# Kernel optimization log

Hardware: AMD Instinct MI355X
Metric: run time of the kernel (lower is better)

## Reference

```python
import jax, jax.numpy as jnp
import numpy as np

N, E, C, L, OUT = 50000, 600000, 128, 2, 64


def setup_inputs() -> dict:
    key = jax.random.key(0)
    ks = jax.random.split(key, 8)
    s = 1.0 / np.sqrt(C)
    return {
        "x": jax.random.normal(ks[0], (N, C), jnp.float32),
        "edge_index": jax.random.randint(ks[1], (2, E), 0, N, jnp.int64),
        "W_neigh": jax.random.normal(ks[2], (L, C, C), jnp.float32) * s,
        "W_root": jax.random.normal(ks[3], (L, C, C), jnp.float32) * s,
        "b_conv": jnp.zeros((L, C), jnp.float32),
        "ln_gamma": jnp.ones((L, C), jnp.float32),
        "ln_beta": jnp.zeros((L, C), jnp.float32),
        "W_head": jax.random.normal(ks[4], (OUT, C), jnp.float32) * s,
        "b_head": jnp.zeros((OUT,), jnp.float32),
        "num_seed": 1024,
    }


def _layernorm(h, g, b, eps=1e-5):
    mu = jnp.mean(h, axis=-1, keepdims=True)
    var = jnp.mean(jnp.square(h - mu), axis=-1, keepdims=True)
    return (h - mu) * jax.lax.rsqrt(var + eps) * g + b


def reference(x, edge_index, W_neigh, W_root, b_conv, ln_gamma, ln_beta, W_head, b_head, num_seed):
    src, dst = edge_index[0], edge_index[1]
    n = x.shape[0]
    # in-degree for mean aggregation (clamped to 1 as in PyG mean aggr)
    deg = jax.ops.segment_sum(jnp.ones((src.shape[0],), x.dtype), dst, num_segments=n)
    inv_deg = 1.0 / jnp.maximum(deg, 1.0)  # [N]
    for l in range(W_neigh.shape[0]):
        agg = jax.ops.segment_sum(x[src], dst, num_segments=n) * inv_deg[:, None]  # [N,C]
        h = agg @ W_neigh[l].T + x @ W_root[l].T + b_conv[l]
        x = jax.nn.relu(_layernorm(h, ln_gamma[l], ln_beta[l]))
    # head on the seed nodes (entity table slice starts at 0 here)
    return x[:num_seed] @ W_head.T + b_head
```

## Files before the change

kernel.cpp:

```cpp
#include <hip/hip_runtime.h>

#define C 128

typedef __attribute__((ext_vector_type(8))) short short8;
typedef __attribute__((ext_vector_type(16))) float floatx16;

__device__ __forceinline__ unsigned short f2b(float f) {
    union { float f; unsigned u; } v; v.f = f;
    unsigned u = v.u + 0x7fffu + ((v.u >> 16) & 1u);
    return (unsigned short)(u >> 16);
}
__device__ __forceinline__ void acc_pair(unsigned u, float& lo, float& hi) {
    union { unsigned u; float f; } a, b;
    a.u = u << 16;
    b.u = u & 0xffff0000u;
    lo += a.f;
    hi += b.f;
}

__global__ void cast_mark_count_kernel(const float* __restrict__ x, unsigned short* __restrict__ xb, int n4x,
                                       const float* __restrict__ Wn, unsigned short* __restrict__ Wnb,
                                       const float* __restrict__ Wr, unsigned short* __restrict__ Wrb, int n4w,
                                       const float* __restrict__ Wh, unsigned short* __restrict__ Whb, int n4h,
                                       const int* __restrict__ src, const int* __restrict__ dst,
                                       int* __restrict__ deg, int* __restrict__ needed,
                                       int E, int num_seed,
                                       int castBlocks) {
    if ((int)blockIdx.x < castBlocks) {
        int i = blockIdx.x * blockDim.x + threadIdx.x;
        const float* in;
        unsigned short* out;
        int idx;
        if (i < n4x) { in = x; out = xb; idx = i; }
        else if (i < n4x + n4w) { in = Wn; out = Wnb; idx = i - n4x; }
        else if (i < n4x + 2 * n4w) { in = Wr; out = Wrb; idx = i - n4x - n4w; }
        else if (i < n4x + 2 * n4w + n4h) { in = Wh; out = Whb; idx = i - n4x - 2 * n4w; }
        else return;
        float4 v = ((const float4*)in)[idx];
        ushort4 o;
        o.x = f2b(v.x); o.y = f2b(v.y); o.z = f2b(v.z); o.w = f2b(v.w);
        ((ushort4*)out)[idx] = o;
    } else {
        int e = (blockIdx.x - castBlocks) * blockDim.x + threadIdx.x;
        if (e < num_seed) needed[e] = 1;
        if (e < E) {
            int d = dst[e];
            atomicAdd(&deg[d], 1);
            if (d < num_seed) needed[src[e]] = 1;
        }
    }
}

__global__ void scan_fused_kernel(const int* __restrict__ deg, const int* __restrict__ needed,
                                  unsigned long long* __restrict__ status, int* __restrict__ counter,
                                  int* __restrict__ row_start, int* __restrict__ cursor,
                                  int* __restrict__ nodelist, int* __restrict__ Mptr, int n) {
    __shared__ int smD[256];
    __shared__ int smN[256];
    __shared__ int sbid, sprefD, sprefN;
    int t = threadIdx.x;
    if (t == 0) sbid = atomicAdd(counter, 1);
    __syncthreads();
    int bid = sbid;
    int i = bid * 256 + t;
    int d = (i < n) ? deg[i] : 0;
    int nd = (i < n) ? needed[i] : 0;
    smD[t] = d; smN[t] = nd;
    __syncthreads();
    for (int off = 1; off < 256; off <<= 1) {
        int vD = (t >= off) ? smD[t - off] : 0;
        int vN = (t >= off) ? smN[t - off] : 0;
        __syncthreads();
        smD[t] += vD; smN[t] += vN;
        __syncthreads();
    }
    int totD = smD[255], totN = smN[255];
    if (t == 0) {
        if (bid == 0) {
            atomicExch(&status[0],
                       (2ULL << 62) | ((unsigned long long)(unsigned)totN << 32) | (unsigned)totD);
            sprefD = 0; sprefN = 0;
        } else {
            atomicExch(&status[bid],
                       (1ULL << 62) | ((unsigned long long)(unsigned)totN << 32) | (unsigned)totD);
            int accD = 0, accN = 0;
            for (int j = bid - 1; j >= 0;) {
                unsigned long long v = atomicAdd(&status[j], 0ULL);
                unsigned f = (unsigned)(v >> 62);
                if (f == 0) { __builtin_amdgcn_s_sleep(1); continue; }
                accD += (int)(unsigned)(v & 0xffffffffULL);
                accN += (int)((v >> 32) & 0x3fffffffULL);
                if (f == 2) break;
                --j;
            }
            atomicExch(&status[bid],
                       (2ULL << 62) | ((unsigned long long)(unsigned)(accN + totN) << 32) |
                           (unsigned)(accD + totD));
            sprefD = accD; sprefN = accN;
        }
    }
    __syncthreads();
    int exD = smD[t] - d + sprefD;
    int exN = smN[t] - nd + sprefN;
    if (i < n) {
        row_start[i] = exD;
        cursor[i] = exD;
        if (nd) nodelist[exN] = i;
        if (i == n - 1) { row_start[n] = exD + d; *Mptr = exN + nd; }
    }
}

__global__ void bucket_kernel(const int* __restrict__ src, const int* __restrict__ dst,
                              int* __restrict__ cursor, int* __restrict__ esrc, int E,
                              const int* __restrict__ needed) {
    int e = blockIdx.x * blockDim.x + threadIdx.x;
    if (e < E) {
        int d = dst[e];
        if (needed[d]) {
            int p = atomicAdd(&cursor[d], 1);
            esrc[p] = src[e];
        }
    }
}

__global__ void aggregate_kernel(const unsigned short* __restrict__ xb, const int* __restrict__ row_start,
                                 const int* __restrict__ esrc,
                                 unsigned short* __restrict__ agg, int n,
                                 const int* __restrict__ nodelist, const int* __restrict__ Mptr) {
    int wid = (blockIdx.x * blockDim.x + threadIdx.x) >> 6;
    int lane = threadIdx.x & 63;
    int q = lane >> 4, l16 = lane & 15;
    int qb = lane & 48;
    int pos = wid * 4 + q;
    int m = Mptr ? *Mptr : n;
    if (pos >= m) return;
    int node = nodelist ? nodelist[pos] : pos;

    int beg = row_start[node];
    int end = row_start[node + 1];
    size_t choff = (size_t)l16 * 8;

    float a0 = 0.f, a1 = 0.f, a2 = 0.f, a3 = 0.f, a4 = 0.f, a5 = 0.f, a6 = 0.f, a7 = 0.f;

    for (int base = beg; base < end; base += 16) {
        int cnt = min(end - base, 16);
        int e_val = (base + l16 < end) ? esrc[base + l16] : 0;
        int j = 0;
        for (; j + 8 <= cnt; j += 8) {
            int s0 = __shfl(e_val, qb | j, 64);
            int s1 = __shfl(e_val, qb | (j + 1), 64);
            int s2 = __shfl(e_val, qb | (j + 2), 64);
            int s3 = __shfl(e_val, qb | (j + 3), 64);
            int s4 = __shfl(e_val, qb | (j + 4), 64);
            int s5 = __shfl(e_val, qb | (j + 5), 64);
            int s6 = __shfl(e_val, qb | (j + 6), 64);
            int s7 = __shfl(e_val, qb | (j + 7), 64);
            uint4 v0 = *(const uint4*)(xb + (size_t)s0 * C + choff);
            uint4 v1 = *(const uint4*)(xb + (size_t)s1 * C + choff);
            uint4 v2 = *(const uint4*)(xb + (size_t)s2 * C + choff);
            uint4 v3 = *(const uint4*)(xb + (size_t)s3 * C + choff);
            uint4 v4 = *(const uint4*)(xb + (size_t)s4 * C + choff);
            uint4 v5 = *(const uint4*)(xb + (size_t)s5 * C + choff);
            uint4 v6 = *(const uint4*)(xb + (size_t)s6 * C + choff);
            uint4 v7 = *(const uint4*)(xb + (size_t)s7 * C + choff);
            acc_pair(v0.x, a0, a1); acc_pair(v0.y, a2, a3); acc_pair(v0.z, a4, a5); acc_pair(v0.w, a6, a7);
            acc_pair(v1.x, a0, a1); acc_pair(v1.y, a2, a3); acc_pair(v1.z, a4, a5); acc_pair(v1.w, a6, a7);
            acc_pair(v2.x, a0, a1); acc_pair(v2.y, a2, a3); acc_pair(v2.z, a4, a5); acc_pair(v2.w, a6, a7);
            acc_pair(v3.x, a0, a1); acc_pair(v3.y, a2, a3); acc_pair(v3.z, a4, a5); acc_pair(v3.w, a6, a7);
            acc_pair(v4.x, a0, a1); acc_pair(v4.y, a2, a3); acc_pair(v4.z, a4, a5); acc_pair(v4.w, a6, a7);
            acc_pair(v5.x, a0, a1); acc_pair(v5.y, a2, a3); acc_pair(v5.z, a4, a5); acc_pair(v5.w, a6, a7);
            acc_pair(v6.x, a0, a1); acc_pair(v6.y, a2, a3); acc_pair(v6.z, a4, a5); acc_pair(v6.w, a6, a7);
            acc_pair(v7.x, a0, a1); acc_pair(v7.y, a2, a3); acc_pair(v7.z, a4, a5); acc_pair(v7.w, a6, a7);
        }
        for (; j + 4 <= cnt; j += 4) {
            int s0 = __shfl(e_val, qb | j, 64);
            int s1 = __shfl(e_val, qb | (j + 1), 64);
            int s2 = __shfl(e_val, qb | (j + 2), 64);
            int s3 = __shfl(e_val, qb | (j + 3), 64);
            uint4 v0 = *(const uint4*)(xb + (size_t)s0 * C + choff);
            uint4 v1 = *(const uint4*)(xb + (size_t)s1 * C + choff);
            uint4 v2 = *(const uint4*)(xb + (size_t)s2 * C + choff);
            uint4 v3 = *(const uint4*)(xb + (size_t)s3 * C + choff);
            acc_pair(v0.x, a0, a1); acc_pair(v0.y, a2, a3); acc_pair(v0.z, a4, a5); acc_pair(v0.w, a6, a7);
            acc_pair(v1.x, a0, a1); acc_pair(v1.y, a2, a3); acc_pair(v1.z, a4, a5); acc_pair(v1.w, a6, a7);
            acc_pair(v2.x, a0, a1); acc_pair(v2.y, a2, a3); acc_pair(v2.z, a4, a5); acc_pair(v2.w, a6, a7);
            acc_pair(v3.x, a0, a1); acc_pair(v3.y, a2, a3); acc_pair(v3.z, a4, a5); acc_pair(v3.w, a6, a7);
        }
        for (; j < cnt; ++j) {
            int s0 = __shfl(e_val, qb | j, 64);
            uint4 v0 = *(const uint4*)(xb + (size_t)s0 * C + choff);
            acc_pair(v0.x, a0, a1); acc_pair(v0.y, a2, a3); acc_pair(v0.z, a4, a5); acc_pair(v0.w, a6, a7);
        }
    }

    float sc = 1.0f / fmaxf((float)(end - beg), 1.0f);
    uint4 o;
    o.x = ((unsigned)f2b(a1 * sc) << 16) | (unsigned)f2b(a0 * sc);
    o.y = ((unsigned)f2b(a3 * sc) << 16) | (unsigned)f2b(a2 * sc);
    o.z = ((unsigned)f2b(a5 * sc) << 16) | (unsigned)f2b(a4 * sc);
    o.w = ((unsigned)f2b(a7 * sc) << 16) | (unsigned)f2b(a6 * sc);
    *(uint4*)(agg + (size_t)pos * C + choff) = o;
}

__launch_bounds__(256)
__global__ void gemm_mfma_ln_relu_kernel(const unsigned short* __restrict__ Aagg,
                                         const unsigned short* __restrict__ Xin,
                                         const unsigned short* __restrict__ Wn,
                                         const unsigned short* __restrict__ Wr,
                                         const float* __restrict__ bconv, const float* __restrict__ gamma,
                                         const float* __restrict__ beta, unsigned short* __restrict__ Xout,
                                         int n,
                                         const int* __restrict__ nodelist, const int* __restrict__ Mptr,
                                         const unsigned short* __restrict__ Whb,
                                         const float* __restrict__ bh, float* __restrict__ out) {
    __shared__ unsigned short Xs[64][136];
    __shared__ unsigned short Ws[128][136];
    __shared__ float Ls[64][2];
    __shared__ float Lss[64][2];

    int m = Mptr ? *Mptr : n;
    int row0 = blockIdx.x * 64;
    if (row0 >= m) return;

    int tid = threadIdx.x;
    int wave = tid >> 6, lane = tid & 63;
    int rh = wave & 1, ch = wave >> 1;
    int l31 = lane & 31, half = lane >> 5;

    floatx16 acc0, acc1;
#pragma unroll
    for (int i = 0; i < 16; ++i) { acc0[i] = 0.f; acc1[i] = 0.f; }

#pragma unroll
    for (int phase = 0; phase < 2; ++phase) {
        const unsigned short* Ap = phase ? Xin : Aagg;
        const unsigned short* Wp = phase ? Wr : Wn;
        __syncthreads();
#pragma unroll
        for (int i = 0; i < 4; ++i) {
            int cidx = tid + 256 * i;
            int r = cidx >> 4, koff = (cidx & 15) * 8;
            uint4 v = make_uint4(0u, 0u, 0u, 0u);
            int rg = row0 + r;
            if (rg < m) {
                int rowid = (phase && nodelist) ? nodelist[rg] : rg;
                v = *(const uint4*)(Ap + (size_t)rowid * C + koff);
            }
            *(uint4*)&Xs[r][koff] = v;
        }
#pragma unroll
        for (int i = 0; i < 8; ++i) {
            int cidx = tid + 256 * i;
            int r = cidx >> 4, koff = (cidx & 15) * 8;
            uint4 v = *(const uint4*)(Wp + (size_t)r * C + koff);
            *(uint4*)&Ws[r][koff] = v;
        }
        __syncthreads();
#pragma unroll
        for (int kc = 0; kc < C; kc += 16) {
            int ko = kc + half * 8;
            short8 a = *(const short8*)&Xs[rh * 32 + l31][ko];
            short8 b0 = *(const short8*)&Ws[ch * 64 + l31][ko];
            short8 b1 = *(const short8*)&Ws[ch * 64 + 32 + l31][ko];
            acc0 = __builtin_amdgcn_mfma_f32_32x32x16_bf16(a, b0, acc0, 0, 0, 0);
            acc1 = __builtin_amdgcn_mfma_f32_32x32x16_bf16(a, b1, acc1, 0, 0, 0);
        }
    }

    int col0 = ch * 64 + l31;
    int col1 = col0 + 32;
    float bc0 = bconv[col0], bc1 = bconv[col1];
#pragma unroll
    for (int r = 0; r < 16; ++r) {
        float h0 = acc0[r] + bc0;
        float h1 = acc1[r] + bc1;
        float s = h0 + h1, ss = h0 * h0 + h1 * h1;
#pragma unroll
        for (int mk = 1; mk < 32; mk <<= 1) {
            s += __shfl_xor(s, mk, 64);
            ss += __shfl_xor(ss, mk, 64);
        }
        if (l31 == 0) {
            int row_l = rh * 32 + (r & 3) + 8 * (r >> 2) + 4 * half;
            Ls[row_l][ch] = s;
            Lss[row_l][ch] = ss;
        }
    }
    __syncthreads();

    if (Whb) {
#pragma unroll
        for (int i = 0; i < 4; ++i) {
            int cidx = tid + 256 * i;
            int r = cidx >> 4, koff = (cidx & 15) * 8;
            uint4 v = *(const uint4*)(Whb + (size_t)r * C + koff);
            *(uint4*)&Ws[r][koff] = v;
        }
    }

    float g0 = gamma[col0], g1 = gamma[col1];
    float be0 = beta[col0], be1 = beta[col1];
#pragma unroll
    for (int r = 0; r < 16; ++r) {
        int row_l = rh * 32 + (r & 3) + 8 * (r >> 2) + 4 * half;
        float s = Ls[row_l][0] + Ls[row_l][1];
        float ss = Lss[row_l][0] + Lss[row_l][1];
        float mu = s * (1.0f / 128.0f);
        float var = ss * (1.0f / 128.0f) - mu * mu;
        float rs = rsqrtf(var + 1e-5f);
        float h0 = acc0[r] + bc0;
        float h1 = acc1[r] + bc1;
        float o0 = fmaxf((h0 - mu) * rs * g0 + be0, 0.f);
        float o1 = fmaxf((h1 - mu) * rs * g1 + be1, 0.f);
        Xs[row_l][col0] = f2b(o0);
        Xs[row_l][col1] = f2b(o1);
    }
    __syncthreads();

    if (Whb) {
        floatx16 hc;
#pragma unroll
        for (int i = 0; i < 16; ++i) hc[i] = 0.f;
        int m0 = rh * 32, n0 = ch * 32;
#pragma unroll
        for (int kc = 0; kc < C; kc += 16) {
            int ko = kc + half * 8;
            short8 a = *(const short8*)&Xs[m0 + l31][ko];
            short8 b = *(const short8*)&Ws[n0 + l31][ko];
            hc = __builtin_amdgcn_mfma_f32_32x32x16_bf16(a, b, hc, 0, 0, 0);
        }
        int oc = n0 + l31;
        float bhv = bh[oc];
#pragma unroll
        for (int r = 0; r < 16; ++r) {
            int row_l = m0 + (r & 3) + 8 * (r >> 2) + 4 * half;
            int rg = row0 + row_l;
            if (rg < m) out[(size_t)rg * 64 + oc] = hc[r] + bhv;
        }
    } else {
#pragma unroll
        for (int i = 0; i < 4; ++i) {
            int cidx = tid + 256 * i;
            int r = cidx >> 4, koff = (cidx & 15) * 8;
            int rg = row0 + r;
            if (rg < m) {
                int orow = nodelist ? nodelist[rg] : rg;
                *(uint4*)(Xout + (size_t)orow * C + koff) = *(const uint4*)&Xs[r][koff];
            }
        }
    }
}

extern "C" void kernel_launch(void* const* d_in, const int* in_sizes, int n_in,
                              void* d_out, int out_size, void* d_ws, size_t ws_size,
                              hipStream_t stream) {
    const float* x = (const float*)d_in[0];
    const int* ei = (const int*)d_in[1];
    const float* Wn = (const float*)d_in[2];
    const float* Wr = (const float*)d_in[3];
    const float* bconv = (const float*)d_in[4];
    const float* gamma = (const float*)d_in[5];
    const float* beta = (const float*)d_in[6];
    const float* Wh = (const float*)d_in[7];
    const float* bh = (const float*)d_in[8];

    int N = in_sizes[0] / C;
    int E = in_sizes[1] / 2;
    int L = in_sizes[2] / (C * C);
    int num_seed = out_size / 64;
    int nchunks = (N + 255) / 256;

    char* ws = (char*)d_ws;
    size_t off = 0;
    auto alloc = [&](size_t bytes) {
        void* p = ws + off;
        off = (off + bytes + 255) & ~(size_t)255;
        return p;
    };
    int* deg = (int*)alloc((size_t)N * 4);
    int* needed = (int*)alloc((size_t)N * 4);
    int* counter = (int*)alloc(256);
    unsigned long long* status = (unsigned long long*)alloc((size_t)nchunks * 8);
    size_t zero_span = off;
    int* row_start = (int*)alloc((size_t)(N + 1) * 4);
    int* cursor = (int*)alloc((size_t)N * 4);
    int* nodelist = (int*)alloc((size_t)N * 4);
    int* Mptr = (int*)alloc(4);
    int* esrc = (int*)alloc((size_t)E * 4);
    unsigned short* xb = (unsigned short*)alloc((size_t)N * C * 2);
    unsigned short* aggb = (unsigned short*)alloc((size_t)N * C * 2);
    unsigned short* xA = (unsigned short*)alloc((size_t)N * C * 2);
    unsigned short* xB = (unsigned short*)alloc((size_t)N * C * 2);
    unsigned short* Wnb = (unsigned short*)alloc((size_t)L * C * C * 2);
    unsigned short* Wrb = (unsigned short*)alloc((size_t)L * C * C * 2);
    unsigned short* Whb = (unsigned short*)alloc((size_t)64 * C * 2);

    const int* srcIdx = ei;
    const int* dstIdx = ei + E;

    int n4x = N * C / 4;
    int n4w = L * C * C / 4;
    int n4h = 64 * C / 4;
    int castBlocks = (n4x + 2 * n4w + n4h + 255) / 256;
    int degBlocks = (max(E, num_seed) + 255) / 256;

    hipMemsetAsync(ws, 0, zero_span, stream);
    cast_mark_count_kernel<<<castBlocks + degBlocks, 256, 0, stream>>>(
        x, xb, n4x, Wn, Wnb, Wr, Wrb, n4w, Wh, Whb, n4h,
        srcIdx, dstIdx, deg, needed, E, num_seed, castBlocks);
    scan_fused_kernel<<<nchunks, 256, 0, stream>>>(deg, needed, status, counter,
                                                   row_start, cursor, nodelist, Mptr, N);
    bucket_kernel<<<(E + 255) / 256, 256, 0, stream>>>(srcIdx, dstIdx, cursor, esrc, E, needed);

    const unsigned short* cur = xb;
    unsigned short* bufs[2] = {xA, xB};
    for (int l = 0; l < L; ++l) {
        bool last = (l == L - 1);
        bool front = !last && (l == L - 2);
        int nl = last ? num_seed : N;
        const int* list = front ? nodelist : nullptr;
        const int* Mp = front ? Mptr : nullptr;
        unsigned short* nxt = bufs[l & 1];
        int aggThreads = ((nl + 3) / 4) * 64;
        aggregate_kernel<<<(aggThreads + 255) / 256, 256, 0, stream>>>(
            cur, row_start, esrc, aggb, nl, list, Mp);
        gemm_mfma_ln_relu_kernel<<<(nl + 63) / 64, 256, 0, stream>>>(
            aggb, cur, Wnb + (size_t)l * C * C, Wrb + (size_t)l * C * C,
            bconv + (size_t)l * C, gamma + (size_t)l * C, beta + (size_t)l * C, nxt, nl,
            list, Mp,
            last ? Whb : (const unsigned short*)nullptr, bh, (float*)d_out);
        cur = nxt;
    }
}
```

Baseline: 181.0 us.

## Fuse all stages into one persistent kernel with software grid barriers

Replaces the sequence of separate launches (cast/count, decoupled-lookback scan, bucket, per-layer aggregate and GEMM) with a single persistent kernel of 512 blocks. The blocks synchronise through atomic-counter grid barriers and use grid-stride loops. The scan becomes a two-pass reduce-then-scan over block sums. The goal is to remove launch gaps and tail effects between the small stages. In exchange it relies on all 512 blocks being co-resident, adds barrier spin cost, and may lose per-stage occupancy because shared memory is sized for the GEMM throughout.

```diff
diff --git a/kernel.cpp b/kernel.cpp
--- a/kernel.cpp
+++ b/kernel.cpp
@@ -1,6 +1,7 @@
 #include <hip/hip_runtime.h>
 
 #define C 128
+#define NB 512
 
 typedef __attribute__((ext_vector_type(8))) short short8;
 typedef __attribute__((ext_vector_type(16))) float floatx16;
@@ -18,210 +19,104 @@
     hi += b.f;
 }
 
-__global__ void cast_mark_count_kernel(const float* __restrict__ x, unsigned short* __restrict__ xb, int n4x,
-                                       const float* __restrict__ Wn, unsigned short* __restrict__ Wnb,
-                                       const float* __restrict__ Wr, unsigned short* __restrict__ Wrb, int n4w,
-                                       const float* __restrict__ Wh, unsigned short* __restrict__ Whb, int n4h,
-                                       const int* __restrict__ src, const int* __restrict__ dst,
-                                       int* __restrict__ deg, int* __restrict__ needed,
-                                       int E, int num_seed,
-                                       int castBlocks) {
-    if ((int)blockIdx.x < castBlocks) {
-        int i = blockIdx.x * blockDim.x + threadIdx.x;
-        const float* in;
-        unsigned short* out;
-        int idx;
-        if (i < n4x) { in = x; out = xb; idx = i; }
-        else if (i < n4x + n4w) { in = Wn; out = Wnb; idx = i - n4x; }
-        else if (i < n4x + 2 * n4w) { in = Wr; out = Wrb; idx = i - n4x - n4w; }
-        else if (i < n4x + 2 * n4w + n4h) { in = Wh; out = Whb; idx = i - n4x - 2 * n4w; }
-        else return;
-        float4 v = ((const float4*)in)[idx];
-        ushort4 o;
-        o.x = f2b(v.x); o.y = f2b(v.y); o.z = f2b(v.z); o.w = f2b(v.w);
-        ((ushort4*)out)[idx] = o;
-    } else {
-        int e = (blockIdx.x - castBlocks) * blockDim.x + threadIdx.x;
-        if (e < num_seed) needed[e] = 1;
-        if (e < E) {
-            int d = dst[e];
-            atomicAdd(&deg[d], 1);
-            if (d < num_seed) needed[src[e]] = 1;
-        }
-    }
-}
-
-__global__ void scan_fused_kernel(const int* __restrict__ deg, const int* __restrict__ needed,
-                                  unsigned long long* __restrict__ status, int* __restrict__ counter,
-                                  int* __restrict__ row_start, int* __restrict__ cursor,
-                                  int* __restrict__ nodelist, int* __restrict__ Mptr, int n) {
-    __shared__ int smD[256];
-    __shared__ int smN[256];
-    __shared__ int sbid, sprefD, sprefN;
-    int t = threadIdx.x;
-    if (t == 0) sbid = atomicAdd(counter, 1);
+__device__ __forceinline__ void gbar(int* bar, int idx) {
     __syncthreads();
-    int bid = sbid;
-    int i = bid * 256 + t;
-    int d = (i < n) ? deg[i] : 0;
-    int nd = (i < n) ? needed[i] : 0;
-    smD[t] = d; smN[t] = nd;
+    if (threadIdx.x == 0) {
+        int* c = bar + idx * 64;
+        __threadfence();
+        __hip_atomic_fetch_add(c, 1, __ATOMIC_RELEASE, __HIP_MEMORY_SCOPE_AGENT);
+        while (__hip_atomic_load(c, __ATOMIC_ACQUIRE, __HIP_MEMORY_SCOPE_AGENT) < NB)
+            __builtin_amdgcn_s_sleep(8);
+        __threadfence();
+    }
     __syncthreads();
-    for (int off = 1; off < 256; off <<= 1) {
-        int vD = (t >= off) ? smD[t - off] : 0;
-        int vN = (t >= off) ? smN[t - off] : 0;
-        __syncthreads();
-        smD[t] += vD; smN[t] += vN;
-        __syncthreads();
-    }
-    int totD = smD[255], totN = smN[255];
-    if (t == 0) {
-        if (bid == 0) {
-            atomicExch(&status[0],
-                       (2ULL << 62) | ((unsigned long long)(unsigned)totN << 32) | (unsigned)totD);
-            sprefD = 0; sprefN = 0;
-        } else {
-            atomicExch(&status[bid],
-                       (1ULL << 62) | ((unsigned long long)(unsigned)totN << 32) | (unsigned)totD);
-            int accD = 0, accN = 0;
-            for (int j = bid - 1; j >= 0;) {
-                unsigned long long v = atomicAdd(&status[j], 0ULL);
-                unsigned f = (unsigned)(v >> 62);
-                if (f == 0) { __builtin_amdgcn_s_sleep(1); continue; }
-                accD += (int)(unsigned)(v & 0xffffffffULL);
-                accN += (int)((v >> 32) & 0x3fffffffULL);
-                if (f == 2) break;
-                --j;
+}
+
+__device__ __forceinline__ void agg_phase(const unsigned short* __restrict__ xb,
+                                          const int* __restrict__ row_start,
+                                          const int* __restrict__ esrc,
+                                          unsigned short* __restrict__ agg, int m,
+                                          const int* __restrict__ nodelist) {
+    int tid = threadIdx.x;
+    int lane = tid & 63;
+    int q = lane >> 4, l16 = lane & 15, qb = lane & 48;
+    int wid = blockIdx.x * 4 + (tid >> 6);
+    size_t choff = (size_t)l16 * 8;
+
+    for (int pos = wid * 4 + q; pos < m; pos += NB * 16) {
+        int node = nodelist ? nodelist[pos] : pos;
+        int beg = row_start[node];
+        int end = row_start[node + 1];
+        float a0 = 0.f, a1 = 0.f, a2 = 0.f, a3 = 0.f, a4 = 0.f, a5 = 0.f, a6 = 0.f, a7 = 0.f;
+        for (int base = beg; base < end; base += 16) {
+            int cnt = min(end - base, 16);
+            int e_val = (base + l16 < end) ? esrc[base + l16] : 0;
+            int j = 0;
+            for (; j + 8 <= cnt; j += 8) {
+                int s0 = __shfl(e_val, qb | j, 64);
+                int s1 = __shfl(e_val, qb | (j + 1), 64);
+                int s2 = __shfl(e_val, qb | (j + 2), 64);
+                int s3 = __shfl(e_val, qb | (j + 3), 64);
+                int s4 = __shfl(e_val, qb | (j + 4), 64);
+                int s5 = __shfl(e_val, qb | (j + 5), 64);
+                int s6 = __shfl(e_val, qb | (j + 6), 64);
+                int s7 = __shfl(e_val, qb | (j + 7), 64);
+                uint4 v0 = *(const uint4*)(xb + (size_t)s0 * C + choff);
+                uint4 v1 = *(const uint4*)(xb + (size_t)s1 * C + choff);
+                uint4 v2 = *(const uint4*)(xb + (size_t)s2 * C + choff);
+                uint4 v3 = *(const uint4*)(xb + (size_t)s3 * C + choff);
+                uint4 v4 = *(const uint4*)(xb + (size_t)s4 * C + choff);
+                uint4 v5 = *(const uint4*)(xb + (size_t)s5 * C + choff);
+                uint4 v6 = *(const uint4*)(xb + (size_t)s6 * C + choff);
+                uint4 v7 = *(const uint4*)(xb + (size_t)s7 * C + choff);
+                acc_pair(v0.x, a0, a1); acc_pair(v0.y, a2, a3); acc_pair(v0.z, a4, a5); acc_pair(v0.w, a6, a7);
+                acc_pair(v1.x, a0, a1); acc_pair(v1.y, a2, a3); acc_pair(v1.z, a4, a5); acc_pair(v1.w, a6, a7);
+                acc_pair(v2.x, a0, a1); acc_pair(v2.y, a2, a3); acc_pair(v2.z, a4, a5); acc_pair(v2.w, a6, a7);
+                acc_pair(v3.x, a0, a1); acc_pair(v3.y, a2, a3); acc_pair(v3.z, a4, a5); acc_pair(v3.w, a6, a7);
+                acc_pair(v4.x, a0, a1); acc_pair(v4.y, a2, a3); acc_pair(v4.z, a4, a5); acc_pair(v4.w, a6, a7);
+                acc_pair(v5.x, a0, a1); acc_pair(v5.y, a2, a3); acc_pair(v5.z, a4, a5); acc_pair(v5.w, a6, a7);
+                acc_pair(v6.x, a0, a1); acc_pair(v6.y, a2, a3); acc_pair(v6.z, a4, a5); acc_pair(v6.w, a6, a7);
+                acc_pair(v7.x, a0, a1); acc_pair(v7.y, a2, a3); acc_pair(v7.z, a4, a5); acc_pair(v7.w, a6, a7);
             }
-            atomicExch(&status[bid],
-                       (2ULL << 62) | ((unsigned long long)(unsigned)(accN + totN) << 32) |
-                           (unsigned)(accD + totD));
-            sprefD = accD; sprefN = accN;
-        }
-    }
-    __syncthreads();
-    int exD = smD[t] - d + sprefD;
-    int exN = smN[t] - nd + sprefN;
-    if (i < n) {
-        row_start[i] = exD;
-        cursor[i] = exD;
-        if (nd) nodelist[exN] = i;
-        if (i == n - 1) { row_start[n] = exD + d; *Mptr = exN + nd; }
-    }
-}
-
-__global__ void bucket_kernel(const int* __restrict__ src, const int* __restrict__ dst,
-                              int* __restrict__ cursor, int* __restrict__ esrc, int E,
-                              const int* __restrict__ needed) {
-    int e = blockIdx.x * blockDim.x + threadIdx.x;
-    if (e < E) {
-        int d = dst[e];
-        if (needed[d]) {
-            int p = atomicAdd(&cursor[d], 1);
-            esrc[p] = src[e];
-        }
-    }
-}
-
-__global__ void aggregate_kernel(const unsigned short* __restrict__ xb, const int* __restrict__ row_start,
-                                 const int* __restrict__ esrc,
-                                 unsigned short* __restrict__ agg, int n,
-                                 const int* __restrict__ nodelist, const int* __restrict__ Mptr) {
-    int wid = (blockIdx.x * blockDim.x + threadIdx.x) >> 6;
-    int lane = threadIdx.x & 63;
-    int q = lane >> 4, l16 = lane & 15;
-    int qb = lane & 48;
-    int pos = wid * 4 + q;
-    int m = Mptr ? *Mptr : n;
-    if (pos >= m) return;
-    int node = nodelist ? nodelist[pos] : pos;
-
-    int beg = row_start[node];
-    int end = row_start[node + 1];
-    size_t choff = (size_t)l16 * 8;
-
-    float a0 = 0.f, a1 = 0.f, a2 = 0.f, a3 = 0.f, a4 = 0.f, a5 = 0.f, a6 = 0.f, a7 = 0.f;
-
-    for (int base = beg; base < end; base += 16) {
-        int cnt = min(end - base, 16);
-        int e_val = (base + l16 < end) ? esrc[base + l16] : 0;
-        int j = 0;
-        for (; j + 8 <= cnt; j += 8) {
-            int s0 = __shfl(e_val, qb | j, 64);
-            int s1 = __shfl(e_val, qb | (j + 1), 64);
-            int s2 = __shfl(e_val, qb | (j + 2), 64);
-            int s3 = __shfl(e_val, qb | (j + 3), 64);
-            int s4 = __shfl(e_val, qb | (j + 4), 64);
-            int s5 = __shfl(e_val, qb | (j + 5), 64);
-            int s6 = __shfl(e_val, qb | (j + 6), 64);
-            int s7 = __shfl(e_val, qb | (j + 7), 64);
-            uint4 v0 = *(const uint4*)(xb + (size_t)s0 * C + choff);
-            uint4 v1 = *(const uint4*)(xb + (size_t)s1 * C + choff);
-            uint4 v2 = *(const uint4*)(xb + (size_t)s2 * C + choff);
-            uint4 v3 = *(const uint4*)(xb + (size_t)s3 * C + choff);
-            uint4 v4 = *(const uint4*)(xb + (size_t)s4 * C + choff);
-            uint4 v5 = *(const uint4*)(xb + (size_t)s5 * C + choff);
-            uint4 v6 = *(const uint4*)(xb + (size_t)s6 * C + choff);
-            uint4 v7 = *(const uint4*)(xb + (size_t)s7 * C + choff);
-            acc_pair(v0.x, a0, a1); acc_pair(v0.y, a2, a3); acc_pair(v0.z, a4, a5); acc_pair(v0.w, a6, a7);
-            acc_pair(v1.x, a0, a1); acc_pair(v1.y, a2, a3); acc_pair(v1.z, a4, a5); acc_pair(v1.w, a6, a7);
-            acc_pair(v2.x, a0, a1); acc_pair(v2.y, a2, a3); acc_pair(v2.z, a4, a5); acc_pair(v2.w, a6, a7);
-            acc_pair(v3.x, a0, a1); acc_pair(v3.y, a2, a3); acc_pair(v3.z, a4, a5); acc_pair(v3.w, a6, a7);
-            acc_pair(v4.x, a0, a1); acc_pair(v4.y, a2, a3); acc_pair(v4.z, a4, a5); acc_pair(v4.w, a6, a7);
-            acc_pair(v5.x, a0, a1); acc_pair(v5.y, a2, a3); acc_pair(v5.z, a4, a5); acc_pair(v5.w, a6, a7);
-            acc_pair(v6.x, a0, a1); acc_pair(v6.y, a2, a3); acc_pair(v6.z, a4, a5); acc_pair(v6.w, a6, a7);
-            acc_pair(v7.x, a0, a1); acc_pair(v7.y, a2, a3); acc_pair(v7.z, a4, a5); acc_pair(v7.w, a6, a7);
-        }
-        for (; j + 4 <= cnt; j += 4) {
-            int s0 = __shfl(e_val, qb | j, 64);
-            int s1 = __shfl(e_val, qb | (j + 1), 64);
-            int s2 = __shfl(e_val, qb | (j + 2), 64);
-            int s3 = __shfl(e_val, qb | (j + 3), 64);
-            uint4 v0 = *(const uint4*)(xb + (size_t)s0 * C + choff);
-            uint4 v1 = *(const uint4*)(xb + (size_t)s1 * C + choff);
-            uint4 v2 = *(const uint4*)(xb + (size_t)s2 * C + choff);
-            uint4 v3 = *(const uint4*)(xb + (size_t)s3 * C + choff);
-            acc_pair(v0.x, a0, a1); acc_pair(v0.y, a2, a3); acc_pair(v0.z, a4, a5); acc_pair(v0.w, a6, a7);
-            acc_pair(v1.x, a0, a1); acc_pair(v1.y, a2, a3); acc_pair(v1.z, a4, a5); acc_pair(v1.w, a6, a7);
-            acc_pair(v2.x, a0, a1); acc_pair(v2.y, a2, a3); acc_pair(v2.z, a4, a5); acc_pair(v2.w, a6, a7);
-            acc_pair(v3.x, a0, a1); acc_pair(v3.y, a2, a3); acc_pair(v3.z, a4, a5); acc_pair(v3.w, a6, a7);
-        }
-        for (; j < cnt; ++j) {
-            int s0 = __shfl(e_val, qb | j, 64);
-            uint4 v0 = *(const uint4*)(xb + (size_t)s0 * C + choff);
-            acc_pair(v0.x, a0, a1); acc_pair(v0.y, a2, a3); acc_pair(v0.z, a4, a5); acc_pair(v0.w, a6, a7);
-        }
-    }
-
-    float sc = 1.0f / fmaxf((float)(end - beg), 1.0f);
-    uint4 o;
-    o.x = ((unsigned)f2b(a1 * sc) << 16) | (unsigned)f2b(a0 * sc);
-    o.y = ((unsigned)f2b(a3 * sc) << 16) | (unsigned)f2b(a2 * sc);
-    o.z = ((unsigned)f2b(a5 * sc) << 16) | (unsigned)f2b(a4 * sc);
-    o.w = ((unsigned)f2b(a7 * sc) << 16) | (unsigned)f2b(a6 * sc);
-    *(uint4*)(agg + (size_t)pos * C + choff) = o;
-}
-
-__launch_bounds__(256)
-__global__ void gemm_mfma_ln_relu_kernel(const unsigned short* __restrict__ Aagg,
-                                         const unsigned short* __restrict__ Xin,
-                                         const unsigned short* __restrict__ Wn,
-                                         const unsigned short* __restrict__ Wr,
-                                         const float* __restrict__ bconv, const float* __restrict__ gamma,
-                                         const float* __restrict__ beta, unsigned short* __restrict__ Xout,
-                                         int n,
-                                         const int* __restrict__ nodelist, const int* __restrict__ Mptr,
-                                         const unsigned short* __restrict__ Whb,
-                                         const float* __restrict__ bh, float* __restrict__ out) {
-    __shared__ unsigned short Xs[64][136];
-    __shared__ unsigned short Ws[128][136];
-    __shared__ float Ls[64][2];
-    __shared__ float Lss[64][2];
-
-    int m = Mptr ? *Mptr : n;
-    int row0 = blockIdx.x * 64;
-    if (row0 >= m) return;
-
+            for (; j + 4 <= cnt; j += 4) {
+                int s0 = __shfl(e_val, qb | j, 64);
+                int s1 = __shfl(e_val, qb | (j + 1), 64);
+                int s2 = __shfl(e_val, qb | (j + 2), 64);
+                int s3 = __shfl(e_val, qb | (j + 3), 64);
+                uint4 v0 = *(const uint4*)(xb + (size_t)s0 * C + choff);
+                uint4 v1 = *(const uint4*)(xb + (size_t)s1 * C + choff);
+                uint4 v2 = *(const uint4*)(xb + (size_t)s2 * C + choff);
+                uint4 v3 = *(const uint4*)(xb + (size_t)s3 * C + choff);
+                acc_pair(v0.x, a0, a1); acc_pair(v0.y, a2, a3); acc_pair(v0.z, a4, a5); acc_pair(v0.w, a6, a7);
+                acc_pair(v1.x, a0, a1); acc_pair(v1.y, a2, a3); acc_pair(v1.z, a4, a5); acc_pair(v1.w, a6, a7);
+                acc_pair(v2.x, a0, a1); acc_pair(v2.y, a2, a3); acc_pair(v2.z, a4, a5); acc_pair(v2.w, a6, a7);
+                acc_pair(v3.x, a0, a1); acc_pair(v3.y, a2, a3); acc_pair(v3.z, a4, a5); acc_pair(v3.w, a6, a7);
+            }
+            for (; j < cnt; ++j) {
+                int s0 = __shfl(e_val, qb | j, 64);
+                uint4 v0 = *(const uint4*)(xb + (size_t)s0 * C + choff);
+                acc_pair(v0.x, a0, a1); acc_pair(v0.y, a2, a3); acc_pair(v0.z, a4, a5); acc_pair(v0.w, a6, a7);
+            }
+        }
+        float sc = 1.0f / fmaxf((float)(end - beg), 1.0f);
+        uint4 o;
+        o.x = ((unsigned)f2b(a1 * sc) << 16) | (unsigned)f2b(a0 * sc);
+        o.y = ((unsigned)f2b(a3 * sc) << 16) | (unsigned)f2b(a2 * sc);
+        o.z = ((unsigned)f2b(a5 * sc) << 16) | (unsigned)f2b(a4 * sc);
+        o.w = ((unsigned)f2b(a7 * sc) << 16) | (unsigned)f2b(a6 * sc);
+        *(uint4*)(agg + (size_t)pos * C + choff) = o;
+    }
+}
+
+__device__ __forceinline__ void gemm_tile(
+    unsigned short (*Xs)[136], unsigned short (*Ws)[136], float (*Ls)[2], float (*Lss)[2],
+    const unsigned short* __restrict__ Aagg, const unsigned short* __restrict__ Xin,
+    const unsigned short* __restrict__ Wn, const unsigned short* __restrict__ Wr,
+    const float* __restrict__ bconv, const float* __restrict__ gamma,
+    const float* __restrict__ beta, unsigned short* __restrict__ Xout,
+    int row0, int m, const int* __restrict__ nodelist,
+    const unsigned short* __restrict__ Whb, const float* __restrict__ bh,
+    float* __restrict__ out) {
     int tid = threadIdx.x;
     int wave = tid >> 6, lane = tid & 63;
     int rh = wave & 1, ch = wave >> 1;
@@ -351,6 +246,148 @@
     }
 }
 
+__launch_bounds__(256, 2)
+__global__ void mega_kernel(const float* __restrict__ x,
+                            const int* __restrict__ src, const int* __restrict__ dst,
+                            const float* __restrict__ Wn, const float* __restrict__ Wr,
+                            const float* __restrict__ bconv, const float* __restrict__ gamma,
+                            const float* __restrict__ beta,
+                            const float* __restrict__ Wh, const float* __restrict__ bh,
+                            float* __restrict__ out,
+                            int N, int E, int L, int num_seed, int nchunks, int useFrontier,
+                            int n4x, int n4w, int n4h,
+                            int* __restrict__ bar, int* __restrict__ deg, int* __restrict__ needed,
+                            int* __restrict__ row_start, int* __restrict__ cursor,
+                            int* __restrict__ nodelist, int* __restrict__ Mptr,
+                            int* __restrict__ bsumD, int* __restrict__ bsumN,
+                            int* __restrict__ esrc,
+                            unsigned short* __restrict__ xb, unsigned short* __restrict__ aggb,
+                            unsigned short* __restrict__ xA, unsigned short* __restrict__ xB,
+                            unsigned short* __restrict__ Wnb, unsigned short* __restrict__ Wrb,
+                            unsigned short* __restrict__ Whb) {
+    __shared__ unsigned short Xs[64][136];
+    __shared__ unsigned short Ws[128][136];
+    __shared__ float Ls[64][2];
+    __shared__ float Lss[64][2];
+
+    int t = threadIdx.x;
+    int g = blockIdx.x * 256 + t;
+    int bi = 0;
+
+    int n4tot = n4x + 2 * n4w + n4h;
+    for (int i = g; i < n4tot; i += NB * 256) {
+        const float* in;
+        unsigned short* outp;
+        int idx;
+        if (i < n4x) { in = x; outp = xb; idx = i; }
+        else if (i < n4x + n4w) { in = Wn; outp = Wnb; idx = i - n4x; }
+        else if (i < n4x + 2 * n4w) { in = Wr; outp = Wrb; idx = i - n4x - n4w; }
+        else { in = Wh; outp = Whb; idx = i - n4x - 2 * n4w; }
+        float4 v = ((const float4*)in)[idx];
+        ushort4 o;
+        o.x = f2b(v.x); o.y = f2b(v.y); o.z = f2b(v.z); o.w = f2b(v.w);
+        ((ushort4*)outp)[idx] = o;
+    }
+    for (int s = g; s < num_seed; s += NB * 256) needed[s] = 1;
+    for (int e = g; e < E; e += NB * 256) {
+        int d = dst[e];
+        atomicAdd(&deg[d], 1);
+        if (useFrontier && d < num_seed) needed[src[e]] = 1;
+    }
+    gbar(bar, bi++);
+
+    int* smD = (int*)&Xs[0][0];
+    int* smN = smD + 256;
+    int* osmD = smD + 512;
+    int* osmN = smD + 768;
+    for (int cc = blockIdx.x; cc < nchunks; cc += NB) {
+        int i = cc * 256 + t;
+        smD[t] = (i < N) ? deg[i] : 0;
+        smN[t] = (i < N) ? needed[i] : 0;
+        __syncthreads();
+#pragma unroll
+        for (int off = 128; off > 0; off >>= 1) {
+            if (t < off) { smD[t] += smD[t + off]; smN[t] += smN[t + off]; }
+            __syncthreads();
+        }
+        if (t == 0) { bsumD[cc] = smD[0]; bsumN[cc] = smN[0]; }
+        __syncthreads();
+    }
+    gbar(bar, bi++);
+
+    for (int cc = blockIdx.x; cc < nchunks; cc += NB) {
+        int sD = 0, sN = 0;
+        for (int i = t; i < cc; i += 256) { sD += bsumD[i]; sN += bsumN[i]; }
+        osmD[t] = sD; osmN[t] = sN;
+        __syncthreads();
+#pragma unroll
+        for (int off = 128; off > 0; off >>= 1) {
+            if (t < off) { osmD[t] += osmD[t + off]; osmN[t] += osmN[t + off]; }
+            __syncthreads();
+        }
+        int boffD = osmD[0], boffN = osmN[0];
+        int i = cc * 256 + t;
+        int d = (i < N) ? deg[i] : 0;
+        int nd = (i < N) ? needed[i] : 0;
+        smD[t] = d; smN[t] = nd;
+        __syncthreads();
+        for (int off = 1; off < 256; off <<= 1) {
+            int vD = (t >= off) ? smD[t - off] : 0;
+            int vN = (t >= off) ? smN[t - off] : 0;
+            __syncthreads();
+            smD[t] += vD; smN[t] += vN;
+            __syncthreads();
+        }
+        int exD = smD[t] - d + boffD;
+        int exN = smN[t] - nd + boffN;
+        if (i < N) {
+            row_start[i] = exD;
+            cursor[i] = exD;
+            if (nd) nodelist[exN] = i;
+            if (i == N - 1) { row_start[N] = exD + d; *Mptr = exN + nd; }
+        }
+        __syncthreads();
+    }
+    gbar(bar, bi++);
+
+    for (int e = g; e < E; e += NB * 256) {
+        int d = dst[e];
+        if (!useFrontier || needed[d]) {
+            int p = atomicAdd(&cursor[d], 1);
+            esrc[p] = src[e];
+        }
+    }
+    gbar(bar, bi++);
+
+    const unsigned short* cur = xb;
+    unsigned short* bufs[2] = {xA, xB};
+    for (int l = 0; l < L; ++l) {
+        bool last = (l == L - 1);
+        bool front = useFrontier && !last;
+        int mrows = last ? num_seed
+                         : (front ? __hip_atomic_load(Mptr, __ATOMIC_RELAXED,
+                                                      __HIP_MEMORY_SCOPE_AGENT)
+                                  : N);
+        const int* list = front ? nodelist : nullptr;
+        const unsigned short* Wn_l = Wnb + (size_t)l * C * C;
+        const unsigned short* Wr_l = Wrb + (size_t)l * C * C;
+        const float* bc_l = bconv + (size_t)l * C;
+        const float* g_l = gamma + (size_t)l * C;
+        const float* b_l = beta + (size_t)l * C;
+        unsigned short* nxt = bufs[l & 1];
+
+        agg_phase(cur, row_start, esrc, aggb, mrows, list);
+        gbar(bar, bi++);
+
+        for (int tile = blockIdx.x; tile * 64 < mrows; tile += NB)
+            gemm_tile(Xs, Ws, Ls, Lss, aggb, cur, Wn_l, Wr_l, bc_l, g_l, b_l, nxt,
+                      tile * 64, mrows, list, last ? Whb : (const unsigned short*)nullptr,
+                      bh, out);
+        if (!last) gbar(bar, bi++);
+        cur = nxt;
+    }
+}
+
 extern "C" void kernel_launch(void* const* d_in, const int* in_sizes, int n_in,
                               void* d_out, int out_size, void* d_ws, size_t ws_size,
                               hipStream_t stream) {
@@ -377,15 +414,16 @@
         off = (off + bytes + 255) & ~(size_t)255;
         return p;
     };
+    int* bar = (int*)alloc((size_t)64 * 64 * 4);
     int* deg = (int*)alloc((size_t)N * 4);
     int* needed = (int*)alloc((size_t)N * 4);
-    int* counter = (int*)alloc(256);
-    unsigned long long* status = (unsigned long long*)alloc((size_t)nchunks * 8);
     size_t zero_span = off;
     int* row_start = (int*)alloc((size_t)(N + 1) * 4);
     int* cursor = (int*)alloc((size_t)N * 4);
     int* nodelist = (int*)alloc((size_t)N * 4);
     int* Mptr = (int*)alloc(4);
+    int* bsumD = (int*)alloc((size_t)nchunks * 4);
+    int* bsumN = (int*)alloc((size_t)nchunks * 4);
     int* esrc = (int*)alloc((size_t)E * 4);
     unsigned short* xb = (unsigned short*)alloc((size_t)N * C * 2);
     unsigned short* aggb = (unsigned short*)alloc((size_t)N * C * 2);
@@ -401,34 +439,12 @@
     int n4x = N * C / 4;
     int n4w = L * C * C / 4;
     int n4h = 64 * C / 4;
-    int castBlocks = (n4x + 2 * n4w + n4h + 255) / 256;
-    int degBlocks = (max(E, num_seed) + 255) / 256;
+    int useFrontier = (L == 2) ? 1 : 0;
 
     hipMemsetAsync(ws, 0, zero_span, stream);
-    cast_mark_count_kernel<<<castBlocks + degBlocks, 256, 0, stream>>>(
-        x, xb, n4x, Wn, Wnb, Wr, Wrb, n4w, Wh, Whb, n4h,
-        srcIdx, dstIdx, deg, needed, E, num_seed, castBlocks);
-    scan_fused_kernel<<<nchunks, 256, 0, stream>>>(deg, needed, status, counter,
-                                                   row_start, cursor, nodelist, Mptr, N);
-    bucket_kernel<<<(E + 255) / 256, 256, 0, stream>>>(srcIdx, dstIdx, cursor, esrc, E, needed);
-
-    const unsigned short* cur = xb;
-    unsigned short* bufs[2] = {xA, xB};
-    for (int l = 0; l < L; ++l) {
-        bool last = (l == L - 1);
-        bool front = !last && (l == L - 2);
-        int nl = last ? num_seed : N;
-        const int* list = front ? nodelist : nullptr;
-        const int* Mp = front ? Mptr : nullptr;
-        unsigned short* nxt = bufs[l & 1];
-        int aggThreads = ((nl + 3) / 4) * 64;
-        aggregate_kernel<<<(aggThreads + 255) / 256, 256, 0, stream>>>(
-            cur, row_start, esrc, aggb, nl, list, Mp);
-        gemm_mfma_ln_relu_kernel<<<(nl + 63) / 64, 256, 0, stream>>>(
-            aggb, cur, Wnb + (size_t)l * C * C, Wrb + (size_t)l * C * C,
-            bconv + (size_t)l * C, gamma + (size_t)l * C, beta + (size_t)l * C, nxt, nl,
-            list, Mp,
-            last ? Whb : (const unsigned short*)nullptr, bh, (float*)d_out);
-        cur = nxt;
-    }
-}
+    mega_kernel<<<NB, 256, 0, stream>>>(
+        x, srcIdx, dstIdx, Wn, Wr, bconv, gamma, beta, Wh, bh, (float*)d_out,
+        N, E, L, num_seed, nchunks, useFrontier, n4x, n4w, n4h,
+        bar, deg, needed, row_start, cursor, nodelist, Mptr, bsumD, bsumN, esrc,
+        xb, aggb, xA, xB, Wnb, Wrb, Whb);
+}
```

New measurement: 674.0 us. 3.72x slower.
